# Kernel optimization log

Measured on AMD Instinct MI355X. Metric: run time of the kernel, lower is better.

## Reference

```python
import jax, jax.numpy as jnp
import numpy as np

N_QUBITS = 12
N_LAYERS = 6
BATCH = 8192
D_IN = 512


def _apply_1q(state, gate, wire):
    # state: [B] + [2]*n (real), gate: [2,2]. new[j] = sum_i gate[j,i]*old[i]
    s = jnp.moveaxis(state, 1 + wire, -1)
    s = jnp.einsum('...i,ji->...j', s, gate)
    return jnp.moveaxis(s, -1, 1 + wire)


def _apply_cnot(state, ctrl, tgt):
    # flip target amplitude pair where control bit == 1
    s = jnp.moveaxis(state, (1 + ctrl, 1 + tgt), (-2, -1))
    s = jnp.concatenate([s[..., :1, :], s[..., 1:, ::-1]], axis=-2)
    return jnp.moveaxis(s, (-2, -1), (1 + ctrl, 1 + tgt))


def _simulate(angles, weights):
    # angles: [B, n] per-sample RY angles; weights: [L, n] shared RY angles.
    # Circuit: H + RY(angle) per wire on |0>, then L x (RY layer + CNOT chain).
    # All gates are real -> real float32 statevector.
    B, n = angles.shape
    L = weights.shape[0]
    inv_sqrt2 = jnp.float32(1.0 / np.sqrt(2.0))
    half = 0.5 * angles
    c, s = jnp.cos(half), jnp.sin(half)
    # per-wire single-qubit state RY(a) @ H @ |0> = inv_sqrt2 * [c-s, c+s]
    v = inv_sqrt2 * jnp.stack([c - s, c + s], axis=-1)  # [B, n, 2]
    state = v[:, 0]  # [B, 2]
    for w in range(1, n):
        state = jnp.einsum('b...,bj->b...j', state, v[:, w])  # product state
    # state: [B] + [2]*n
    for layer in range(L):
        h = 0.5 * weights[layer]
        cl, sl = jnp.cos(h), jnp.sin(h)
        for w in range(n):
            gate = jnp.stack([jnp.stack([cl[w], -sl[w]]),
                              jnp.stack([sl[w], cl[w]])])
            state = _apply_1q(state, gate, w)
        for w in range(n - 1):
            state = _apply_cnot(state, w, w + 1)
    probs = state * state
    zs = []
    for w in range(n):
        axes = tuple(a for a in range(1, n + 1) if a != 1 + w)
        p = probs.sum(axis=axes)  # [B, 2]
        zs.append(p[:, 0] - p[:, 1])
    return jnp.stack(zs, axis=-1)  # [B, n] = <Z_i>


def setup_inputs() -> dict:
    key = jax.random.key(0)
    ks = jax.random.split(key, 6)
    x = jax.random.normal(ks[0], (BATCH, D_IN), jnp.float32)
    pre_w = jax.random.normal(ks[1], (N_QUBITS, D_IN), jnp.float32) / np.sqrt(D_IN)
    pre_b = jax.random.normal(ks[2], (N_QUBITS,), jnp.float32) * 0.01
    weights = jax.random.normal(ks[3], (N_LAYERS, N_QUBITS), jnp.float32)
    post_w = jax.random.normal(ks[4], (1, N_QUBITS), jnp.float32) / np.sqrt(N_QUBITS)
    post_b = jax.random.normal(ks[5], (1,), jnp.float32) * 0.01
    return {"x": x, "pre_w": pre_w, "pre_b": pre_b, "weights": weights,
            "post_w": post_w, "post_b": post_b}


def reference(x, pre_w, pre_b, weights, post_w, post_b):
    pre = x @ pre_w.T + pre_b                # [B, n_qubits]
    angles = pre * jnp.float32(np.pi / 2.0)  # RY(inputs[i]*pi/2)
    q_out = _simulate(angles, weights)       # [B, n_qubits]
    return q_out @ post_w.T + post_b         # [B, 1]
```

## Files before the change

### kernel.cpp

```cpp
#include <hip/hip_runtime.h>
#include <math.h>

#define NQ 12
#define NL 6
#define BATCHN 8192
#define DIN 512

typedef _Float16 f16;
typedef __attribute__((ext_vector_type(8)))  _Float16 f16x8;
typedef __attribute__((ext_vector_type(16))) float    f32x16;
typedef unsigned int u32;
typedef __attribute__((ext_vector_type(4))) u32 u32x4;


__device__ __forceinline__ u32 pkrtz(float a, float b) {
  auto p = __builtin_amdgcn_cvt_pkrtz(a, b);
  return __builtin_bit_cast(u32, p);
}
__device__ __forceinline__ u32 bperm(int addr, u32 v) {
  return (u32)__builtin_amdgcn_ds_bpermute(addr, (int)v);
}
__device__ __forceinline__ float dppx1(float v) {
  return __int_as_float(__builtin_amdgcn_mov_dpp(__float_as_int(v), 0xB1, 0xF, 0xF, true));
}
__device__ __forceinline__ float dppx2(float v) {
  return __int_as_float(__builtin_amdgcn_mov_dpp(__float_as_int(v), 0x4E, 0xF, 0xF, true));
}
__device__ __forceinline__ float dppx8(float v) {
  return __int_as_float(__builtin_amdgcn_mov_dpp(__float_as_int(v), 0x128, 0xF, 0xF, true));
}
template <int PAT>
__device__ __forceinline__ float swzf(float v) {
  return __int_as_float(__builtin_amdgcn_ds_swizzle(__float_as_int(v), PAT));
}
__device__ __forceinline__ float wave_sum(float v) {
  v += dppx1(v);
  v += dppx2(v);
  v += swzf<0x101F>(v);
  v += dppx8(v);
  v += swzf<0x401F>(v);
  v += __shfl_xor(v, 32, 64);
  return v;
}
__device__ __forceinline__ f16x8 asf(const u32 a[4]) {
  u32x4 v; v.x = a[0]; v.y = a[1]; v.z = a[2]; v.w = a[3];
  return __builtin_bit_cast(f16x8, v);
}
__device__ __forceinline__ f16x8 ldB(const u32* __restrict__ p, int off) {
  u32x4 v = *(const u32x4*)(p + off);
  return __builtin_bit_cast(f16x8, v);
}

__global__ void setup_mats(const float* __restrict__ weights, u32* __restrict__ Bbuf) {
  const int mm = blockIdx.x >> 3;
  const int l  = mm >> 1;
  const int qs = mm & 1;
  __shared__ float c6[6], s6[6];
  if (threadIdx.x < 6) {
    float h = 0.5f * weights[l * NQ + qs * 6 + threadIdx.x];
    c6[threadIdx.x] = cosf(h);
    s6[threadIdx.x] = sinf(h);
  }
  __syncthreads();
  const int t = (blockIdx.x & 7) * 256 + threadIdx.x;
  const int lane = (t >> 2) & 63;
  const int fk   = t >> 8;
  const int kt   = fk & 3;
  const int nt   = fk >> 2;
  const int n     = nt * 32 + (lane & 31);
  const int kbase = kt * 16 + (lane >> 5) * 8 + (t & 3) * 2;
  float v[2];
  #pragma unroll
  for (int u = 0; u < 2; ++u) {
    int k = kbase + u;
    int bb = k;
    if (l >= 1) { bb ^= bb << 1; bb ^= bb << 2; bb ^= bb << 4; bb &= 63; }
    float prod = 1.f;
    #pragma unroll
    for (int w = 0; w < 6; ++w) {
      const int aw = (n >> w) & 1, bw = (bb >> w) & 1;
      prod *= (aw == bw) ? c6[w] : (aw ? s6[w] : -s6[w]);
    }
    v[u] = prod;
  }
  Bbuf[mm * 2048 + t] = pkrtz(v[0], v[1]);
}

__device__ __forceinline__ void mm_step(f32x16 (&d)[2][2], const u32* __restrict__ Bl,
                                        bool hi, int axor) {
  u32 fr[2][4][4];
  #pragma unroll
  for (int kt = 0; kt < 4; ++kt) {
    const int s  = kt >> 1;
    const int b0 = 4 * ((2 * kt) & 3);
    const int b1 = 4 * ((2 * kt + 1) & 3);
    #pragma unroll
    for (int mt = 0; mt < 2; ++mt) {
      u32 p0a = pkrtz(d[s][mt][b0 + 0], d[s][mt][b0 + 1]);
      u32 p0b = pkrtz(d[s][mt][b0 + 2], d[s][mt][b0 + 3]);
      u32 p1a = pkrtz(d[s][mt][b1 + 0], d[s][mt][b1 + 1]);
      u32 p1b = pkrtz(d[s][mt][b1 + 2], d[s][mt][b1 + 3]);
      u32 x0a = bperm(axor, p0a), x0b = bperm(axor, p0b);
      u32 x1a = bperm(axor, p1a), x1b = bperm(axor, p1b);
      fr[mt][kt][0] = hi ? x1a : p0a;
      fr[mt][kt][1] = hi ? x1b : p0b;
      fr[mt][kt][2] = hi ? p1a : x0a;
      fr[mt][kt][3] = hi ? p1b : x0b;
    }
  }
  #pragma unroll
  for (int kt = 0; kt < 4; ++kt) {
    f16x8 A0 = asf(fr[0][kt]);
    f16x8 A1 = asf(fr[1][kt]);
    f16x8 B0 = ldB(Bl, (0 * 4 + kt) * 256);
    f16x8 B1 = ldB(Bl, (1 * 4 + kt) * 256);
    if (kt == 0) {
      f32x16 z{};
      d[0][0] = __builtin_amdgcn_mfma_f32_32x32x16_f16(A0, B0, z, 0, 0, 0);
      d[0][1] = __builtin_amdgcn_mfma_f32_32x32x16_f16(A0, B1, z, 0, 0, 0);
      d[1][0] = __builtin_amdgcn_mfma_f32_32x32x16_f16(A1, B0, z, 0, 0, 0);
      d[1][1] = __builtin_amdgcn_mfma_f32_32x32x16_f16(A1, B1, z, 0, 0, 0);
    } else {
      d[0][0] = __builtin_amdgcn_mfma_f32_32x32x16_f16(A0, B0, d[0][0], 0, 0, 0);
      d[0][1] = __builtin_amdgcn_mfma_f32_32x32x16_f16(A0, B1, d[0][1], 0, 0, 0);
      d[1][0] = __builtin_amdgcn_mfma_f32_32x32x16_f16(A1, B0, d[1][0], 0, 0, 0);
      d[1][1] = __builtin_amdgcn_mfma_f32_32x32x16_f16(A1, B1, d[1][1], 0, 0, 0);
    }
  }
}

__device__ __forceinline__ void flip_step(f32x16 (&d)[2][2], bool hi) {
  #pragma unroll
  for (int mt = 0; mt < 2; ++mt)
    #pragma unroll
    for (int nt = 0; nt < 2; ++nt)
      #pragma unroll
      for (int r = 0; r < 16; ++r) {
        const int par0 = (__builtin_popcount(r & 3) + __builtin_popcount(r >> 2) + mt) & 1;
        float cur = d[mt][nt][r];
        float partner = dppx1(cur);
        const bool cond = par0 ? !hi : hi;
        d[mt][nt][r] = cond ? partner : cur;
      }
}

__global__ void __launch_bounds__(256) __attribute__((amdgpu_waves_per_eu(3, 4)))
dqc_main(const float* __restrict__ x,
         const float* __restrict__ pre_w,
         const float* __restrict__ pre_b,
         const float* __restrict__ post_w,
         const float* __restrict__ post_b,
         const u32* __restrict__ Bbuf,
         float* __restrict__ out)
{
  const int lane = threadIdx.x & 63;
  const bool hi  = lane >= 32;
  const int b    = blockIdx.x * 4 + (threadIdx.x >> 6);
  const int axor = (lane ^ 32) << 2;

  float acc[NQ];
  const float* xr = x + (size_t)b * DIN + lane * 8;
  const float4 xa = *(const float4*)(xr);
  const float4 xb = *(const float4*)(xr + 4);
  #pragma unroll
  for (int w = 0; w < NQ; ++w) {
    const float* wr = pre_w + w * DIN + lane * 8;
    const float4 wa = *(const float4*)(wr);
    const float4 wb = *(const float4*)(wr + 4);
    acc[w] = xa.x * wa.x + xa.y * wa.y + xa.z * wa.z + xa.w * wa.w
           + xb.x * wb.x + xb.y * wb.y + xb.z * wb.z + xb.w * wb.w;
  }
  #pragma unroll
  for (int w = 0; w < NQ; ++w) acc[w] = wave_sum(acc[w]);

  const float PI_4 = 0.78539816339744830962f;
  const float INV_SQRT2 = 0.70710678118654752440f;
  float v0[NQ], v1[NQ];
  #pragma unroll
  for (int w = 0; w < NQ; ++w) {
    float h = (acc[w] + pre_b[w]) * PI_4;
    float s, c;
    sincosf(h, &s, &c);
    v0[w] = (c - s) * INV_SQRT2;
    v1[w] = (c + s) * INV_SQRT2;
  }

  float base8[8];
  #pragma unroll
  for (int j = 0; j < 8; ++j)
    base8[j] = ((j & 1) ? v1[0] : v0[0]) * ((j & 2) ? v1[1] : v0[1]) * ((j & 4) ? v1[2] : v0[2]);
  float hiP[4];
  #pragma unroll
  for (int kt = 0; kt < 4; ++kt)
    hiP[kt] = (hi ? v1[3] : v0[3]) * ((kt & 1) ? v1[4] : v0[4]) * ((kt & 2) ? v1[5] : v0[5]);
  const float qb = ((lane & 1) ? v1[6] : v0[6]) * ((lane & 2) ? v1[7] : v0[7])
                 * ((lane & 4) ? v1[8] : v0[8]) * ((lane & 8) ? v1[9] : v0[9])
                 * ((lane & 16) ? v1[10] : v0[10]);
  const float qm0 = qb * v0[11], qm1 = qb * v1[11];

  f32x16 d[2][2];
  {
    const u32* Bl = Bbuf + lane * 4;
    #pragma unroll
    for (int kt = 0; kt < 4; ++kt) {
      u32 a0[4], a1[4];
      #pragma unroll
      for (int dw = 0; dw < 4; ++dw) {
        const float e0 = base8[2 * dw] * hiP[kt];
        const float e1 = base8[2 * dw + 1] * hiP[kt];
        a0[dw] = pkrtz(qm0 * e0, qm0 * e1);
        a1[dw] = pkrtz(qm1 * e0, qm1 * e1);
      }
      f16x8 A0 = asf(a0), A1 = asf(a1);
      f16x8 B0 = ldB(Bl, (0 * 4 + kt) * 256);
      f16x8 B1 = ldB(Bl, (1 * 4 + kt) * 256);
      if (kt == 0) {
        f32x16 z{};
        d[0][0] = __builtin_amdgcn_mfma_f32_32x32x16_f16(A0, B0, z, 0, 0, 0);
        d[0][1] = __builtin_amdgcn_mfma_f32_32x32x16_f16(A0, B1, z, 0, 0, 0);
        d[1][0] = __builtin_amdgcn_mfma_f32_32x32x16_f16(A1, B0, z, 0, 0, 0);
        d[1][1] = __builtin_amdgcn_mfma_f32_32x32x16_f16(A1, B1, z, 0, 0, 0);
      } else {
        d[0][0] = __builtin_amdgcn_mfma_f32_32x32x16_f16(A0, B0, d[0][0], 0, 0, 0);
        d[0][1] = __builtin_amdgcn_mfma_f32_32x32x16_f16(A0, B1, d[0][1], 0, 0, 0);
        d[1][0] = __builtin_amdgcn_mfma_f32_32x32x16_f16(A1, B0, d[1][0], 0, 0, 0);
        d[1][1] = __builtin_amdgcn_mfma_f32_32x32x16_f16(A1, B1, d[1][1], 0, 0, 0);
      }
    }
  }

  #pragma clang loop unroll(disable)
  for (int t = 1; t < 12; ++t) {
    mm_step(d, Bbuf + t * 2048 + lane * 4, hi, axor);
    if (t & 1) flip_step(d, hi);
  }

  float tot = 0.f, s0 = 0.f;
  float zp0 = 0.f, zp1 = 0.f, zp3 = 0.f, zp4 = 0.f, zp5 = 0.f;
  #pragma unroll
  for (int mt = 0; mt < 2; ++mt)
    #pragma unroll
    for (int nt = 0; nt < 2; ++nt)
      #pragma unroll
      for (int r = 0; r < 16; ++r) {
        float v = d[mt][nt][r];
        float sq = v * v;
        tot += sq;
        if (nt == 0) s0 += sq;
        const int c0 = r & 1;
        const int c1 = (r ^ (r >> 1)) & 1;
        const int c3 = c1 ^ ((r >> 2) & 1);
        const int c4 = c3 ^ ((r >> 3) & 1);
        const int c5 = c4 ^ mt;
        zp0 += c0 ? -sq : sq;
        zp1 += c1 ? -sq : sq;
        zp3 += c3 ? -sq : sq;
        zp4 += c4 ? -sq : sq;
        zp5 += c5 ? -sq : sq;
      }
  const float sgnhi = hi ? -1.f : 1.f;
  float z[12];
  z[0] = zp0;
  z[1] = zp1;
  z[2] = sgnhi * zp1;
  z[3] = sgnhi * zp3;
  z[4] = sgnhi * zp4;
  z[5] = sgnhi * zp5;
  #pragma unroll
  for (int j = 0; j < 5; ++j) {
    const int par = __builtin_popcount(lane & ((2 << j) - 1)) & 1;
    z[6 + j] = par ? -tot : tot;
  }
  {
    const int par = __builtin_popcount(lane & 31) & 1;
    z[11] = (par ? -1.f : 1.f) * (2.f * s0 - tot);
  }
  const float tots = wave_sum(tot);
  #pragma unroll
  for (int w = 0; w < 12; ++w) z[w] = wave_sum(z[w]);

  if (lane == 0) {
    const float inv = 1.0f / tots;
    float o = post_b[0];
    #pragma unroll
    for (int w = 0; w < 12; ++w) o = fmaf(z[w] * inv, post_w[w], o);
    out[b] = o;
  }
}

extern "C" void kernel_launch(void* const* d_in, const int* in_sizes, int n_in,
                              void* d_out, int out_size, void* d_ws, size_t ws_size,
                              hipStream_t stream) {
  (void)in_sizes; (void)n_in; (void)out_size; (void)ws_size;
  const float* x       = (const float*)d_in[0];
  const float* pre_w   = (const float*)d_in[1];
  const float* pre_b   = (const float*)d_in[2];
  const float* weights = (const float*)d_in[3];
  const float* post_w  = (const float*)d_in[4];
  const float* post_b  = (const float*)d_in[5];
  float* out = (float*)d_out;
  u32* Bbuf = (u32*)d_ws;

  setup_mats<<<96, 256, 0, stream>>>(weights, Bbuf);
  dqc_main<<<BATCHN / 4, 256, 0, stream>>>(x, pre_w, pre_b, post_w, post_b, Bbuf, out);
}
```

Baseline: 138.3 us.

## Fold CNOT flip into packed fp16 operands and use permlane32 swap

Removes the separate per-element DPP flip pass over the f32 accumulators. The flip is now applied on the packed fp16 words inside the next matmul step, using a masked DPP select, and the final flip is handled by rewriting the Z-expectation parity formulas. The cross-half operand exchange now uses permlane32_swap instead of ds_bpermute plus selects when the builtin is available. The occupancy hint also changes to 4 waves per EU, which may affect register allocation.

```diff
diff --git a/kernel.cpp b/kernel.cpp
--- a/kernel.cpp
+++ b/kernel.cpp
@@ -11,6 +11,7 @@
 typedef __attribute__((ext_vector_type(16))) float    f32x16;
 typedef unsigned int u32;
 typedef __attribute__((ext_vector_type(4))) u32 u32x4;
+typedef __attribute__((ext_vector_type(2))) int i32x2;
 
 
 __device__ __forceinline__ u32 pkrtz(float a, float b) {
@@ -22,6 +23,9 @@
 }
 __device__ __forceinline__ float dppx1(float v) {
   return __int_as_float(__builtin_amdgcn_mov_dpp(__float_as_int(v), 0xB1, 0xF, 0xF, true));
+}
+__device__ __forceinline__ u32 dppx1u(u32 v) {
+  return (u32)__builtin_amdgcn_mov_dpp((int)v, 0xB1, 0xF, 0xF, true);
 }
 __device__ __forceinline__ float dppx2(float v) {
   return __int_as_float(__builtin_amdgcn_mov_dpp(__float_as_int(v), 0x4E, 0xF, 0xF, true));
@@ -49,6 +53,26 @@
 __device__ __forceinline__ f16x8 ldB(const u32* __restrict__ p, int off) {
   u32x4 v = *(const u32x4*)(p + off);
   return __builtin_bit_cast(f16x8, v);
+}
+
+#if __has_builtin(__builtin_amdgcn_permlane32_swap)
+__device__ __forceinline__ void pswap(u32& a, u32& b) {
+  i32x2 r = __builtin_amdgcn_permlane32_swap((int)a, (int)b, false, false);
+  a = (u32)r.x; b = (u32)r.y;
+}
+#else
+#define PSWAP_FALLBACK 1
+__device__ __forceinline__ void pswap_fb(u32& a, u32& b, bool hi, int axor) {
+  u32 xa = bperm(axor, a), xb = bperm(axor, b);
+  u32 na = hi ? xb : a;
+  u32 nb = hi ? b : xa;
+  a = na; b = nb;
+}
+#endif
+
+__device__ __forceinline__ u32 foldw(u32 w, u32 m) {
+  u32 partner = dppx1u(w);
+  return (m & partner) | (~m & w);
 }
 
 __global__ void setup_mats(const float* __restrict__ weights, u32* __restrict__ Bbuf) {
@@ -86,8 +110,9 @@
   Bbuf[mm * 2048 + t] = pkrtz(v[0], v[1]);
 }
 
+template <bool FOLD>
 __device__ __forceinline__ void mm_step(f32x16 (&d)[2][2], const u32* __restrict__ Bl,
-                                        bool hi, int axor) {
+                                        bool hi, int axor, u32 maskA, u32 maskB) {
   u32 fr[2][4][4];
   #pragma unroll
   for (int kt = 0; kt < 4; ++kt) {
@@ -100,12 +125,26 @@
       u32 p0b = pkrtz(d[s][mt][b0 + 2], d[s][mt][b0 + 3]);
       u32 p1a = pkrtz(d[s][mt][b1 + 0], d[s][mt][b1 + 1]);
       u32 p1b = pkrtz(d[s][mt][b1 + 2], d[s][mt][b1 + 3]);
-      u32 x0a = bperm(axor, p0a), x0b = bperm(axor, p0b);
-      u32 x1a = bperm(axor, p1a), x1b = bperm(axor, p1b);
-      fr[mt][kt][0] = hi ? x1a : p0a;
-      fr[mt][kt][1] = hi ? x1b : p0b;
-      fr[mt][kt][2] = hi ? p1a : x0a;
-      fr[mt][kt][3] = hi ? p1b : x0b;
+      if (FOLD) {
+        const int PAR4[4] = {0, 1, 1, 0};
+        const int ka = (PAR4[b0 >> 2] + s) & 1;
+        const int kc = (PAR4[b1 >> 2] + s) & 1;
+        p0a = foldw(p0a, ka ? maskB : maskA);
+        p0b = foldw(p0b, ka ? maskA : maskB);
+        p1a = foldw(p1a, kc ? maskB : maskA);
+        p1b = foldw(p1b, kc ? maskA : maskB);
+      }
+#ifdef PSWAP_FALLBACK
+      pswap_fb(p0a, p1a, hi, axor);
+      pswap_fb(p0b, p1b, hi, axor);
+#else
+      pswap(p0a, p1a);
+      pswap(p0b, p1b);
+#endif
+      fr[mt][kt][0] = p0a;
+      fr[mt][kt][1] = p0b;
+      fr[mt][kt][2] = p1a;
+      fr[mt][kt][3] = p1b;
     }
   }
   #pragma unroll
@@ -129,22 +168,7 @@
   }
 }
 
-__device__ __forceinline__ void flip_step(f32x16 (&d)[2][2], bool hi) {
-  #pragma unroll
-  for (int mt = 0; mt < 2; ++mt)
-    #pragma unroll
-    for (int nt = 0; nt < 2; ++nt)
-      #pragma unroll
-      for (int r = 0; r < 16; ++r) {
-        const int par0 = (__builtin_popcount(r & 3) + __builtin_popcount(r >> 2) + mt) & 1;
-        float cur = d[mt][nt][r];
-        float partner = dppx1(cur);
-        const bool cond = par0 ? !hi : hi;
-        d[mt][nt][r] = cond ? partner : cur;
-      }
-}
-
-__global__ void __launch_bounds__(256) __attribute__((amdgpu_waves_per_eu(3, 4)))
+__global__ void __launch_bounds__(256) __attribute__((amdgpu_waves_per_eu(4)))
 dqc_main(const float* __restrict__ x,
          const float* __restrict__ pre_w,
          const float* __restrict__ pre_b,
@@ -157,6 +181,8 @@
   const bool hi  = lane >= 32;
   const int b    = blockIdx.x * 4 + (threadIdx.x >> 6);
   const int axor = (lane ^ 32) << 2;
+  const u32 maskA = hi ? 0x0000FFFFu : 0xFFFF0000u;
+  const u32 maskB = ~maskA;
 
   float acc[NQ];
   const float* xr = x + (size_t)b * DIN + lane * 8;
@@ -230,12 +256,13 @@
   }
 
   #pragma clang loop unroll(disable)
-  for (int t = 1; t < 12; ++t) {
-    mm_step(d, Bbuf + t * 2048 + lane * 4, hi, axor);
-    if (t & 1) flip_step(d, hi);
-  }
-
-  float tot = 0.f, s0 = 0.f;
+  for (int i = 0; i < 5; ++i) {
+    mm_step<false>(d, Bbuf + (2 * i + 1) * 2048 + lane * 4, hi, axor, maskA, maskB);
+    mm_step<true >(d, Bbuf + (2 * i + 2) * 2048 + lane * 4, hi, axor, maskA, maskB);
+  }
+  mm_step<false>(d, Bbuf + 11 * 2048 + lane * 4, hi, axor, maskA, maskB);
+
+  float A0 = 0.f, A1 = 0.f, s00 = 0.f, s01 = 0.f;
   float zp0 = 0.f, zp1 = 0.f, zp3 = 0.f, zp4 = 0.f, zp5 = 0.f;
   #pragma unroll
   for (int mt = 0; mt < 2; ++mt)
@@ -245,8 +272,9 @@
       for (int r = 0; r < 16; ++r) {
         float v = d[mt][nt][r];
         float sq = v * v;
-        tot += sq;
-        if (nt == 0) s0 += sq;
+        const int par0 = (__builtin_popcount(r & 3) + __builtin_popcount(r >> 2) + mt) & 1;
+        if (par0) A1 += sq; else A0 += sq;
+        if (nt == 0) { if (par0) s01 += sq; else s00 += sq; }
         const int c0 = r & 1;
         const int c1 = (r ^ (r >> 1)) & 1;
         const int c3 = c1 ^ ((r >> 2) & 1);
@@ -259,6 +287,9 @@
         zp5 += c5 ? -sq : sq;
       }
   const float sgnhi = hi ? -1.f : 1.f;
+  const float tot   = A0 + A1;
+  const float diff  = sgnhi * (A0 - A1);
+  const float diffs = sgnhi * (2.f * (s00 - s01) - (A0 - A1));
   float z[12];
   z[0] = zp0;
   z[1] = zp1;
@@ -269,11 +300,11 @@
   #pragma unroll
   for (int j = 0; j < 5; ++j) {
     const int par = __builtin_popcount(lane & ((2 << j) - 1)) & 1;
-    z[6 + j] = par ? -tot : tot;
+    z[6 + j] = par ? -diff : diff;
   }
   {
     const int par = __builtin_popcount(lane & 31) & 1;
-    z[11] = (par ? -1.f : 1.f) * (2.f * s0 - tot);
+    z[11] = par ? -diffs : diffs;
   }
   const float tots = wave_sum(tot);
   #pragma unroll
```

New measurement: 129.4 us. 6.4% less time.
